# Kernel optimization log

Measured on AMD Instinct MI355X. Metric: run time of the kernel, lower is better.

The kernel has to match this reference:

```python
import jax, jax.numpy as jnp
import numpy as np

N_NODES = 100000
N_EDGES = 1600000
D_IN, D_HID, D_OUT = 64, 64, 32


def _glorot(key, shape):
    fan_in, fan_out = shape[0], shape[1]
    lim = np.sqrt(6.0 / (fan_in + fan_out)).astype(np.float32)
    return jax.random.uniform(key, shape, jnp.float32, -lim, lim)


def setup_inputs() -> dict:
    key = jax.random.key(0)
    ks = jax.random.split(key, 12)
    x = jax.random.normal(ks[0], (N_NODES, D_IN), jnp.float32)
    edge_index = jax.random.randint(ks[1], (2, N_EDGES), 0, N_NODES, jnp.int64)
    return {
        "x": x,
        "edge_index": edge_index,
        # SAGEConv 1 (in->hid): lin_l (aggregated neighbors, with bias), lin_r (root, no bias)
        "Wl1": _glorot(ks[2], (D_IN, D_HID)),
        "Wr1": _glorot(ks[3], (D_IN, D_HID)),
        "b1": jnp.zeros((D_HID,), jnp.float32),
        # SAGEConv 2 (hid->out)
        "Wl2": _glorot(ks[4], (D_HID, D_OUT)),
        "Wr2": _glorot(ks[5], (D_HID, D_OUT)),
        "b2": jnp.zeros((D_OUT,), jnp.float32),
        # trust head: Linear(32,16) -> ReLU -> Linear(16,1) -> Sigmoid (dropout inert in eval)
        "Wt1": _glorot(ks[6], (D_OUT, 16)),
        "bt1": jnp.zeros((16,), jnp.float32),
        "Wt2": _glorot(ks[7], (16, 1)),
        "bt2": jnp.zeros((1,), jnp.float32),
    }


def _sage_conv(x, src, dst, Wl, Wr, b):
    # mean-aggregate neighbor messages: msg flows src -> dst
    msg = x[src]                                              # [E, d] gather
    agg_sum = jax.ops.segment_sum(msg, dst, num_segments=N_NODES)
    deg = jax.ops.segment_sum(jnp.ones((src.shape[0],), x.dtype), dst,
                              num_segments=N_NODES)
    agg = agg_sum / jnp.maximum(deg, 1.0)[:, None]            # zero-degree -> 0
    return agg @ Wl + x @ Wr + b


def reference(x, edge_index, Wl1, Wr1, b1, Wl2, Wr2, b2, Wt1, bt1, Wt2, bt2):
    src, dst = edge_index[0], edge_index[1]
    h = _sage_conv(x, src, dst, Wl1, Wr1, b1)
    h = jax.nn.relu(h)                    # dropout p=0.3 inert in eval
    h = _sage_conv(h, src, dst, Wl2, Wr2, b2)
    t = jax.nn.relu(h @ Wt1 + bt1)        # dropout p=0.2 inert in eval
    trust = jax.nn.sigmoid(t @ Wt2 + bt2)
    return h, trust
```

## Files before the change

### kernel.cpp

```cpp
#include <hip/hip_runtime.h>
#include <math.h>


#define NBUCK   1563
#define BCAP    1536
#define BKCHUNK 4096

typedef __attribute__((ext_vector_type(8))) __bf16 bf16x8;
typedef __attribute__((ext_vector_type(4))) float  f32x4;

union BU { bf16x8 v; unsigned short u[8]; };

__device__ inline unsigned short f2bf(float x) {
    unsigned u = __float_as_uint(x);
    unsigned r = u + 0x7fffu + ((u >> 16) & 1u);
    return (unsigned short)(r >> 16);
}
__device__ inline unsigned pack2(float a, float b) {
    return (unsigned)f2bf(a) | ((unsigned)f2bf(b) << 16);
}
__device__ inline float bflo(unsigned u) { return __uint_as_float(u << 16); }
__device__ inline float bfhi(unsigned u) { return __uint_as_float(u & 0xffff0000u); }
__device__ inline float bf2f(unsigned short h) { return __uint_as_float((unsigned)h << 16); }

__global__ __launch_bounds__(256) void k_m1(
    const float* __restrict__ x,
    const float* __restrict__ Wl1, const float* __restrict__ Wr1,
    const float* __restrict__ b1,
    unsigned* __restrict__ u16b, float* __restrict__ v,
    const int* __restrict__ src, const int* __restrict__ dst,
    int* __restrict__ gcnt, unsigned* __restrict__ pairs,
    int N, int E, int GB, int BKB)
{
    __shared__ __align__(16) char smem[36864];
    int tid = threadIdx.x;
    int g = blockIdx.x / 5, r5 = blockIdx.x % 5;

    if (r5 == 4) {
        if (g >= BKB) return;
        int* hist = (int*)smem;
        int e0 = g * BKCHUNK;
        int e1 = min(e0 + BKCHUNK, E);

        for (int i = tid; i < NBUCK; i += 256) hist[i] = 0;
        __syncthreads();
        for (int e = e0 + tid; e < e1; e += 256)
            atomicAdd(&hist[((unsigned)dst[e]) >> 6], 1);
        __syncthreads();
        for (int i = tid; i < NBUCK; i += 256)
            if (hist[i] > 0)
                hist[i] = i * BCAP + atomicAdd(&gcnt[i], hist[i]);
        __syncthreads();
        for (int e = e0 + tid; e < e1; e += 256) {
            int t = dst[e];
            int b = ((unsigned)t) >> 6;
            int pos = atomicAdd(&hist[b], 1);
            if (pos < (b + 1) * BCAP)
                pairs[pos] = (unsigned)src[e] | ((unsigned)(t & 63) << 17);
        }
        return;
    }

    int tile = 4 * g + r5;
    if (tile >= GB) return;
    unsigned short* sW = (unsigned short*)smem;
    const int PL = 64 * 72;
    int nblk = tile * 64;

    for (int i = tid * 4; i < 64 * 64; i += 1024) {
        int k = i >> 6, n = i & 63;
        float4 a  = *(const float4*)&Wl1[i];
        float4 bq = *(const float4*)&Wr1[i];
        float av[4] = {a.x, a.y, a.z, a.w};
        float bv[4] = {bq.x, bq.y, bq.z, bq.w};
        #pragma unroll
        for (int j = 0; j < 4; ++j) {
            unsigned short h0 = f2bf(av[j]);
            unsigned short l0 = f2bf(av[j] - bf2f(h0));
            unsigned short h1 = f2bf(bv[j]);
            unsigned short l1 = f2bf(bv[j] - bf2f(h1));
            int o = (n + j) * 72 + k;
            sW[0 * PL + o] = h0; sW[1 * PL + o] = l0;
            sW[2 * PL + o] = h1; sW[3 * PL + o] = l1;
        }
    }
    __syncthreads();

    int l  = tid & 63, wv = tid >> 6;
    int la = l & 15,   g4 = l >> 4;
    int arow = nblk + wv * 16 + la;
    bool rowOK = (arow < N);

    BU ahi[2], alo[2];
    #pragma unroll
    for (int kf = 0; kf < 2; ++kf) {
        float xv[8];
        if (rowOK) {
            const float* xp = &x[(size_t)arow * 64 + kf * 32 + g4 * 8];
            float4 p0 = *(const float4*)xp;
            float4 p1 = *(const float4*)(xp + 4);
            xv[0] = p0.x; xv[1] = p0.y; xv[2] = p0.z; xv[3] = p0.w;
            xv[4] = p1.x; xv[5] = p1.y; xv[6] = p1.z; xv[7] = p1.w;
        } else {
            #pragma unroll
            for (int e = 0; e < 8; ++e) xv[e] = 0.0f;
        }
        #pragma unroll
        for (int e = 0; e < 8; ++e) {
            unsigned short h = f2bf(xv[e]);
            ahi[kf].u[e] = h;
            alo[kf].u[e] = f2bf(xv[e] - bf2f(h));
        }
    }

    unsigned short* u16 = (unsigned short*)u16b;

    #pragma unroll
    for (int pass = 0; pass < 2; ++pass) {
        const unsigned short* Whi = sW + (pass ? 2 : 0) * PL;
        const unsigned short* Wlo = sW + (pass ? 3 : 1) * PL;
        #pragma unroll
        for (int nf = 0; nf < 4; ++nf) {
            int n0 = nf * 16;
            f32x4 acc = {0.f, 0.f, 0.f, 0.f};
            #pragma unroll
            for (int kf = 0; kf < 2; ++kf) {
                int off = (n0 + la) * 72 + kf * 32 + g4 * 8;
                bf16x8 bhi = *(const bf16x8*)&Whi[off];
                bf16x8 blo = *(const bf16x8*)&Wlo[off];
                acc = __builtin_amdgcn_mfma_f32_16x16x32_bf16(ahi[kf].v, bhi, acc, 0, 0, 0);
                acc = __builtin_amdgcn_mfma_f32_16x16x32_bf16(alo[kf].v, bhi, acc, 0, 0, 0);
                acc = __builtin_amdgcn_mfma_f32_16x16x32_bf16(ahi[kf].v, blo, acc, 0, 0, 0);
            }
            if (pass == 0) {
                #pragma unroll
                for (int r = 0; r < 4; ++r) {
                    int nd = nblk + wv * 16 + g4 * 4 + r;
                    if (nd < N)
                        u16[(size_t)nd * 64 + n0 + la] = f2bf(acc[r]);
                }
            } else {
                float bb = b1[n0 + la];
                #pragma unroll
                for (int r = 0; r < 4; ++r) {
                    int nd = nblk + wv * 16 + g4 * 4 + r;
                    if (nd < N)
                        v[(size_t)nd * 64 + n0 + la] = acc[r] + bb;
                }
            }
        }
    }
}

__global__ __launch_bounds__(512) void k_m2(
    const unsigned* __restrict__ pairs, const int* __restrict__ gcnt,
    const unsigned* __restrict__ u16b, const float* __restrict__ v,
    const float* __restrict__ Wl2, const float* __restrict__ Wr2,
    const float* __restrict__ b2,
    unsigned* __restrict__ P16b, float* __restrict__ Qout,
    int2* __restrict__ nodeOff, int* __restrict__ adjG, int N)
{
    __shared__ float sH[64 * 66];
    __shared__ float sW[64 * 64];
    __shared__ int   sAdj[BCAP];
    __shared__ int   sOff[65];
    __shared__ int   sCur[64];
    int tid = threadIdx.x;
    int b = blockIdx.x;
    int nodeBase = b * 64;
    int base = b * BCAP;
    int count = min(gcnt[b], BCAP);
    const unsigned* pp = pairs + (size_t)b * BCAP;

    for (int i = tid * 4; i < 64 * 64; i += 2048) {
        int k = i >> 6, n = i & 63;
        const float* Wsrc = (n < 32) ? (Wl2 + k * 32 + n) : (Wr2 + k * 32 + (n - 32));
        *(float4*)&sW[k * 64 + n] = *(const float4*)Wsrc;
    }
    if (tid < 64) sCur[tid] = 0;
    __syncthreads();

    for (int j = tid; j < count; j += 512)
        atomicAdd(&sCur[(pp[j] >> 17) & 63], 1);
    __syncthreads();
    if (tid < 64) {
        int c = sCur[tid];
        int incl = c;
        #pragma unroll
        for (int off = 1; off < 64; off <<= 1) {
            int t = __shfl_up(incl, off);
            if (tid >= off) incl += t;
        }
        sOff[tid] = incl - c;
        if (tid == 63) sOff[64] = incl;
    }
    __syncthreads();
    if (tid < 64) {
        sCur[tid] = sOff[tid];
        int node = nodeBase + tid;
        if (node < N)
            nodeOff[node] = make_int2(base + sOff[tid], sOff[tid + 1] - sOff[tid]);
    }
    __syncthreads();
    for (int j = tid; j < count; j += 512) {
        unsigned e = pp[j];
        int pos = atomicAdd(&sCur[(e >> 17) & 63], 1);
        sAdj[pos] = (int)(e & 0x1FFFFu);
    }
    __syncthreads();
    for (int j = tid; j < count; j += 512) adjG[base + j] = sAdj[j];

    int hw = tid >> 5, lane = tid & 31;
    for (int r = 0; r < 4; ++r) {
        int nl = hw * 4 + r;
        int node = nodeBase + nl;
        float h0 = 0.0f, h1v = 0.0f;
        if (node < N) {
            int beg = sOff[nl], end = sOff[nl + 1];
            float lo[8] = {0,0,0,0,0,0,0,0}, hi[8] = {0,0,0,0,0,0,0,0};
            int i = beg;
            for (; i + 8 <= end; i += 8) {
                int s[8];
                #pragma unroll
                for (int j = 0; j < 8; ++j) s[j] = sAdj[i + j];
                #pragma unroll
                for (int j = 0; j < 8; ++j) {
                    unsigned w = u16b[(size_t)s[j] * 32 + lane];
                    lo[j] += bflo(w); hi[j] += bfhi(w);
                }
            }
            for (; i < end; ++i) {
                unsigned w = u16b[(size_t)sAdj[i] * 32 + lane];
                lo[0] += bflo(w); hi[0] += bfhi(w);
            }
            float mlo = ((lo[0]+lo[1])+(lo[2]+lo[3])) + ((lo[4]+lo[5])+(lo[6]+lo[7]));
            float mhi = ((hi[0]+hi[1])+(hi[2]+hi[3])) + ((hi[4]+hi[5])+(hi[6]+hi[7]));
            int deg = end - beg;
            float invd = (deg > 0) ? 1.0f / (float)deg : 1.0f;
            float2 vv = ((const float2*)v)[(size_t)node * 32 + lane];
            h0  = fmaxf(mlo * invd + vv.x, 0.0f);
            h1v = fmaxf(mhi * invd + vv.y, 0.0f);
        }
        *(float2*)&sH[nl * 66 + 2 * lane] = make_float2(h0, h1v);
    }
    __syncthreads();

    int ng = tid & 15;
    int mg = tid >> 4;
    int m0 = mg * 2, n0 = ng * 4;

    float acc[2][4];
    #pragma unroll
    for (int mi = 0; mi < 2; ++mi)
        #pragma unroll
        for (int ni = 0; ni < 4; ++ni) acc[mi][ni] = 0.0f;

    #pragma unroll 8
    for (int k = 0; k < 64; ++k) {
        float a0 = sH[(m0 + 0) * 66 + k];
        float a1 = sH[(m0 + 1) * 66 + k];
        float4 w = *(float4*)&sW[k * 64 + n0];
        float wv[4] = {w.x, w.y, w.z, w.w};
        #pragma unroll
        for (int ni = 0; ni < 4; ++ni) {
            acc[0][ni] = fmaf(a0, wv[ni], acc[0][ni]);
            acc[1][ni] = fmaf(a1, wv[ni], acc[1][ni]);
        }
    }

    if (n0 < 32) {
        #pragma unroll
        for (int mi = 0; mi < 2; ++mi) {
            int node = nodeBase + m0 + mi;
            if (node >= N) continue;
            uint2 pk;
            pk.x = pack2(acc[mi][0], acc[mi][1]);
            pk.y = pack2(acc[mi][2], acc[mi][3]);
            *(uint2*)&P16b[(size_t)node * 16 + (n0 >> 1)] = pk;
        }
    } else {
        float4 b0 = *(const float4*)&b2[n0 - 32];
        #pragma unroll
        for (int mi = 0; mi < 2; ++mi) {
            int node = nodeBase + m0 + mi;
            if (node >= N) continue;
            *(float4*)&Qout[(size_t)node * 32 + (n0 - 32)] =
                make_float4(acc[mi][0]+b0.x, acc[mi][1]+b0.y,
                            acc[mi][2]+b0.z, acc[mi][3]+b0.w);
        }
    }
}

__global__ __launch_bounds__(256) void k_a2(
    const int2* __restrict__ nodeOff, const int* __restrict__ adj,
    const unsigned* __restrict__ P16b, const float* __restrict__ Q,
    const float* __restrict__ Wt1, const float* __restrict__ bt1,
    const float* __restrict__ Wt2, const float* __restrict__ bt2,
    float* __restrict__ out_h, float* __restrict__ out_trust, int N)
{
    __shared__ float sWt1[32 * 16];
    __shared__ float sWt2[16];
    for (int i = threadIdx.x; i < 512; i += 256) sWt1[i] = Wt1[i];
    if (threadIdx.x < 16) sWt2[threadIdx.x] = Wt2[threadIdx.x];
    __syncthreads();

    int n = blockIdx.x * 16 + (threadIdx.x >> 4);
    int lane = threadIdx.x & 15;
    if (n >= N) return;

    int2 od = nodeOff[n];
    int beg = od.x, end = od.x + od.y;
    float lo[8] = {0,0,0,0,0,0,0,0}, hi[8] = {0,0,0,0,0,0,0,0};
    int i = beg;
    for (; i + 8 <= end; i += 8) {
        int s[8];
        #pragma unroll
        for (int j = 0; j < 8; ++j) s[j] = adj[i + j];
        #pragma unroll
        for (int j = 0; j < 8; ++j) {
            unsigned w = P16b[(size_t)s[j] * 16 + lane];
            lo[j] += bflo(w); hi[j] += bfhi(w);
        }
    }
    for (; i < end; ++i) {
        unsigned w = P16b[(size_t)adj[i] * 16 + lane];
        lo[0] += bflo(w); hi[0] += bfhi(w);
    }
    float invd = (od.y > 0) ? 1.0f / (float)od.y : 1.0f;
    float mlo = (((lo[0]+lo[1])+(lo[2]+lo[3])) + ((lo[4]+lo[5])+(lo[6]+lo[7]))) * invd;
    float mhi = (((hi[0]+hi[1])+(hi[2]+hi[3])) + ((hi[4]+hi[5])+(hi[6]+hi[7]))) * invd;

    float2 qv = ((const float2*)Q)[(size_t)n * 16 + lane];
    float hx = mlo + qv.x;
    float hy = mhi + qv.y;

    ((float2*)out_h)[(size_t)n * 16 + lane] = make_float2(hx, hy);

    float t = bt1[lane];
    #pragma unroll
    for (int k = 0; k < 16; ++k) {
        float hlo = __shfl(hx, k, 16);
        float hhi = __shfl(hy, k, 16);
        t += hlo * sWt1[(2 * k) * 16 + lane] + hhi * sWt1[(2 * k + 1) * 16 + lane];
    }
    t = fmaxf(t, 0.0f);
    float z = t * sWt2[lane];
    z += __shfl_xor(z, 1);
    z += __shfl_xor(z, 2);
    z += __shfl_xor(z, 4);
    z += __shfl_xor(z, 8);
    if (lane == 0) out_trust[n] = 1.0f / (1.0f + expf(-(z + bt2[0])));
}


extern "C" void kernel_launch(void* const* d_in, const int* in_sizes, int n_in,
                              void* d_out, int out_size, void* d_ws, size_t ws_size,
                              hipStream_t stream)
{
    const float* x   = (const float*)d_in[0];
    const int*   ei  = (const int*)d_in[1];
    const float* Wl1 = (const float*)d_in[2];
    const float* Wr1 = (const float*)d_in[3];
    const float* b1  = (const float*)d_in[4];
    const float* Wl2 = (const float*)d_in[5];
    const float* Wr2 = (const float*)d_in[6];
    const float* b2  = (const float*)d_in[7];
    const float* Wt1 = (const float*)d_in[8];
    const float* bt1 = (const float*)d_in[9];
    const float* Wt2 = (const float*)d_in[10];
    const float* bt2 = (const float*)d_in[11];

    const int N = in_sizes[0] / 64;
    const int E = in_sizes[1] / 2;
    const int* src = ei;
    const int* dst = ei + E;

    unsigned* pairs  = (unsigned*)d_ws;
    unsigned* u16b   = pairs + (size_t)NBUCK * BCAP;
    float*    v      = (float*)(u16b + (size_t)N * 32);
    unsigned* P16b   = (unsigned*)(v + (size_t)N * 64);
    float*    Q      = (float*)(P16b + (size_t)N * 16);
    int2*     nodeOff= (int2*)(Q + (size_t)N * 32);
    int*      adj    = (int*)(nodeOff + N);
    int*      gcnt   = adj + (size_t)NBUCK * BCAP;

    hipMemsetAsync(gcnt, 0, 2048 * sizeof(int), stream);

    const int GB  = (N + 63) / 64;
    const int BKB = (E + BKCHUNK - 1) / BKCHUNK;
    int grp = (GB + 3) / 4 > BKB ? (GB + 3) / 4 : BKB;
    k_m1<<<5 * grp, 256, 0, stream>>>(x, Wl1, Wr1, b1, u16b, v,
                                      src, dst, gcnt, pairs, N, E, GB, BKB);
    k_m2<<<NBUCK, 512, 0, stream>>>(pairs, gcnt, u16b, v, Wl2, Wr2, b2,
                                    P16b, Q, nodeOff, adj, N);

    float* out_h     = (float*)d_out;
    float* out_trust = out_h + (size_t)N * 32;
    k_a2<<<(N + 15) / 16, 256, 0, stream>>>(nodeOff, adj, P16b, Q,
                                            Wt1, bt1, Wt2, bt2,
                                            out_h, out_trust, N);
}
```

Before: 233.0 us.

## Precompute split-bf16 layer-1 weights once in a tiny pre-kernel in fragment layout

Adds a one-block kernel that converts Wl1/Wr1 into hi/lo bf16 pairs laid out per MFMA fragment, so each k_m1 tile block loads its B operands straight from global/L2 instead of rebuilding a 36KB shared-memory copy and syncing. Shared memory in k_m1 shrinks to the histogram only, which may raise occupancy. The bucket-offset reservation loop is also restructured to issue all global atomics before writing back. The cost is an extra kernel launch and per-fragment global loads in the MFMA loop.

```diff
diff --git a/kernel.cpp b/kernel.cpp
--- a/kernel.cpp
+++ b/kernel.cpp
@@ -23,22 +23,48 @@
 __device__ inline float bfhi(unsigned u) { return __uint_as_float(u & 0xffff0000u); }
 __device__ inline float bf2f(unsigned short h) { return __uint_as_float((unsigned)h << 16); }
 
+__global__ __launch_bounds__(256) void k_w(
+    const float* __restrict__ Wl1, const float* __restrict__ Wr1,
+    unsigned short* __restrict__ Wf)
+{
+    int tid = threadIdx.x;
+    for (int idx = tid; idx < 1024; idx += 256) {
+        int q = idx >> 6;
+        int l = idx & 63;
+        int pass = q >> 3, nf = (q >> 1) & 3, kf = q & 1;
+        const float* W = pass ? Wr1 : Wl1;
+        int col  = nf * 16 + (l & 15);
+        int krow = kf * 32 + (l >> 4) * 8;
+        unsigned short hi8[8], lo8[8];
+        #pragma unroll
+        for (int e = 0; e < 8; ++e) {
+            float w = W[(krow + e) * 64 + col];
+            unsigned short h = f2bf(w);
+            hi8[e] = h;
+            lo8[e] = f2bf(w - bf2f(h));
+        }
+        #pragma unroll
+        for (int e = 0; e < 8; ++e) {
+            Wf[(q * 2 + 0) * 512 + l * 8 + e] = hi8[e];
+            Wf[(q * 2 + 1) * 512 + l * 8 + e] = lo8[e];
+        }
+    }
+}
+
 __global__ __launch_bounds__(256) void k_m1(
     const float* __restrict__ x,
-    const float* __restrict__ Wl1, const float* __restrict__ Wr1,
-    const float* __restrict__ b1,
+    const unsigned short* __restrict__ Wf, const float* __restrict__ b1,
     unsigned* __restrict__ u16b, float* __restrict__ v,
     const int* __restrict__ src, const int* __restrict__ dst,
     int* __restrict__ gcnt, unsigned* __restrict__ pairs,
     int N, int E, int GB, int BKB)
 {
-    __shared__ __align__(16) char smem[36864];
+    __shared__ int hist[NBUCK];
     int tid = threadIdx.x;
     int g = blockIdx.x / 5, r5 = blockIdx.x % 5;
 
     if (r5 == 4) {
         if (g >= BKB) return;
-        int* hist = (int*)smem;
         int e0 = g * BKCHUNK;
         int e1 = min(e0 + BKCHUNK, E);
 
@@ -47,9 +73,22 @@
         for (int e = e0 + tid; e < e1; e += 256)
             atomicAdd(&hist[((unsigned)dst[e]) >> 6], 1);
         __syncthreads();
-        for (int i = tid; i < NBUCK; i += 256)
-            if (hist[i] > 0)
-                hist[i] = i * BCAP + atomicAdd(&gcnt[i], hist[i]);
+        int cnt[7], base[7];
+        #pragma unroll
+        for (int t = 0; t < 7; ++t) {
+            int i = tid + t * 256;
+            cnt[t] = (i < NBUCK) ? hist[i] : 0;
+        }
+        #pragma unroll
+        for (int t = 0; t < 7; ++t) {
+            int i = tid + t * 256;
+            base[t] = (i < NBUCK) ? atomicAdd(&gcnt[i], cnt[t]) : 0;
+        }
+        #pragma unroll
+        for (int t = 0; t < 7; ++t) {
+            int i = tid + t * 256;
+            if (i < NBUCK) hist[i] = i * BCAP + base[t];
+        }
         __syncthreads();
         for (int e = e0 + tid; e < e1; e += 256) {
             int t = dst[e];
@@ -63,28 +102,7 @@
 
     int tile = 4 * g + r5;
     if (tile >= GB) return;
-    unsigned short* sW = (unsigned short*)smem;
-    const int PL = 64 * 72;
     int nblk = tile * 64;
-
-    for (int i = tid * 4; i < 64 * 64; i += 1024) {
-        int k = i >> 6, n = i & 63;
-        float4 a  = *(const float4*)&Wl1[i];
-        float4 bq = *(const float4*)&Wr1[i];
-        float av[4] = {a.x, a.y, a.z, a.w};
-        float bv[4] = {bq.x, bq.y, bq.z, bq.w};
-        #pragma unroll
-        for (int j = 0; j < 4; ++j) {
-            unsigned short h0 = f2bf(av[j]);
-            unsigned short l0 = f2bf(av[j] - bf2f(h0));
-            unsigned short h1 = f2bf(bv[j]);
-            unsigned short l1 = f2bf(bv[j] - bf2f(h1));
-            int o = (n + j) * 72 + k;
-            sW[0 * PL + o] = h0; sW[1 * PL + o] = l0;
-            sW[2 * PL + o] = h1; sW[3 * PL + o] = l1;
-        }
-    }
-    __syncthreads();
 
     int l  = tid & 63, wv = tid >> 6;
     int la = l & 15,   g4 = l >> 4;
@@ -117,17 +135,15 @@
 
     #pragma unroll
     for (int pass = 0; pass < 2; ++pass) {
-        const unsigned short* Whi = sW + (pass ? 2 : 0) * PL;
-        const unsigned short* Wlo = sW + (pass ? 3 : 1) * PL;
         #pragma unroll
         for (int nf = 0; nf < 4; ++nf) {
             int n0 = nf * 16;
             f32x4 acc = {0.f, 0.f, 0.f, 0.f};
             #pragma unroll
             for (int kf = 0; kf < 2; ++kf) {
-                int off = (n0 + la) * 72 + kf * 32 + g4 * 8;
-                bf16x8 bhi = *(const bf16x8*)&Whi[off];
-                bf16x8 blo = *(const bf16x8*)&Wlo[off];
+                int q2 = ((pass * 4 + nf) * 2 + kf) * 2;
+                bf16x8 bhi = *(const bf16x8*)&Wf[(q2 + 0) * 512 + l * 8];
+                bf16x8 blo = *(const bf16x8*)&Wf[(q2 + 1) * 512 + l * 8];
                 acc = __builtin_amdgcn_mfma_f32_16x16x32_bf16(ahi[kf].v, bhi, acc, 0, 0, 0);
                 acc = __builtin_amdgcn_mfma_f32_16x16x32_bf16(alo[kf].v, bhi, acc, 0, 0, 0);
                 acc = __builtin_amdgcn_mfma_f32_16x16x32_bf16(ahi[kf].v, blo, acc, 0, 0, 0);
@@ -383,13 +399,16 @@
     int2*     nodeOff= (int2*)(Q + (size_t)N * 32);
     int*      adj    = (int*)(nodeOff + N);
     int*      gcnt   = adj + (size_t)NBUCK * BCAP;
+    unsigned short* Wf = (unsigned short*)(gcnt + 2048);
 
     hipMemsetAsync(gcnt, 0, 2048 * sizeof(int), stream);
+
+    k_w<<<1, 256, 0, stream>>>(Wl1, Wr1, Wf);
 
     const int GB  = (N + 63) / 64;
     const int BKB = (E + BKCHUNK - 1) / BKCHUNK;
     int grp = (GB + 3) / 4 > BKB ? (GB + 3) / 4 : BKB;
-    k_m1<<<5 * grp, 256, 0, stream>>>(x, Wl1, Wr1, b1, u16b, v,
+    k_m1<<<5 * grp, 256, 0, stream>>>(x, Wf, b1, u16b, v,
                                       src, dst, gcnt, pairs, N, E, GB, BKB);
     k_m2<<<NBUCK, 512, 0, stream>>>(pairs, gcnt, u16b, v, Wl2, Wr2, b2,
                                     P16b, Q, nodeOff, adj, N);
```

Result: no change. 231.4 us (-0.7%).
